# Kernel optimization log

Hardware: AMD Instinct MI355X
Metric: run time of the kernel (lower is better)

The kernel has to match this reference:

```python
import jax, jax.numpy as jnp
import numpy as np

N = 20000       # nodes
E = 320000      # edges (before self-loops)
F_IN = 1024     # num_features
H = 4           # head_num
C = 64          # hidden_size
NC = 4          # n_classes
NEG_SLOPE = 0.2 # PyG GATConv default


def setup_inputs() -> dict:
    key = jax.random.key(0)
    ks = jax.random.split(key, 16)
    def w(k, shape, fan_in):
        return jax.random.normal(k, shape, dtype=jnp.float32) / np.sqrt(fan_in)
    x = jax.random.normal(ks[0], (N, F_IN), dtype=jnp.float32)
    edge_index = jax.random.randint(ks[1], (2, E), 0, N, dtype=jnp.int64)
    return {
        "x": x,
        "edge_index": edge_index,
        # layer 1: F_IN -> H*C, concat
        "w1": w(ks[2], (F_IN, H * C), F_IN),
        "as1": w(ks[3], (H, C), C),
        "ad1": w(ks[4], (H, C), C),
        "b1": jnp.zeros((H * C,), jnp.float32),
        # layer 2: H*C -> H*C, concat
        "w2": w(ks[5], (H * C, H * C), H * C),
        "as2": w(ks[6], (H, C), C),
        "ad2": w(ks[7], (H, C), C),
        "b2": jnp.zeros((H * C,), jnp.float32),
        # out layer: H*C -> C, 1 head, concat=False
        "w3": w(ks[8], (H * C, 1 * C), H * C),
        "as3": w(ks[9], (1, C), C),
        "ad3": w(ks[10], (1, C), C),
        "b3": jnp.zeros((C,), jnp.float32),
        # classifier
        "wc": w(ks[11], (C, NC), C),
        "bc": jnp.zeros((NC,), jnp.float32),
    }


def gat_layer(x, src, dst, W, a_src, a_dst, bias, concat):
    """PyG GATConv (eval mode, self-loops already added to src/dst)."""
    n = x.shape[0]
    Hh, Cc = a_src.shape
    h = (x @ W).reshape(n, Hh, Cc)                       # [N,H,C]
    al_s = jnp.sum(h * a_src[None], axis=-1)             # [N,H]
    al_d = jnp.sum(h * a_dst[None], axis=-1)             # [N,H]
    e = al_s[src] + al_d[dst]                            # [E,H]
    e = jax.nn.leaky_relu(e, NEG_SLOPE)
    # segment softmax over incoming edges of each destination node
    emax = jax.ops.segment_max(e, dst, num_segments=n)   # [N,H]
    ex = jnp.exp(e - emax[dst])
    denom = jax.ops.segment_sum(ex, dst, num_segments=n) # [N,H]
    alpha = ex / (denom[dst] + 1e-16)                    # [E,H]
    msg = h[src] * alpha[..., None]                      # [E,H,C]
    out = jax.ops.segment_sum(msg, dst, num_segments=n)  # [N,H,C]
    if concat:
        out = out.reshape(n, Hh * Cc)
    else:
        out = out.mean(axis=1)
    return out + bias


def reference(x, edge_index, w1, as1, ad1, b1, w2, as2, ad2, b2,
              w3, as3, ad3, b3, wc, bc):
    n = x.shape[0]
    loop = jnp.arange(n, dtype=edge_index.dtype)
    src = jnp.concatenate([edge_index[0], loop])
    dst = jnp.concatenate([edge_index[1], loop])
    out = jax.nn.relu(gat_layer(x, src, dst, w1, as1, ad1, b1, True))
    out = jax.nn.relu(gat_layer(out, src, dst, w2, as2, ad2, b2, True))
    out = gat_layer(out, src, dst, w3, as3, ad3, b3, False)
    return out @ wc + bc                                  # [N, n_classes]
```

## Files before the change

### kernel.cpp

```cpp
#include <hip/hip_runtime.h>

#define N_NODES 20000
#define N_EDGES 320000
#define ET (N_EDGES + N_NODES)
#define F_IN 1024
#define HC 256
#define NC 4

typedef unsigned short ushort_t;
typedef __attribute__((ext_vector_type(8))) short short8;
typedef __attribute__((ext_vector_type(4))) float f32x4;

__device__ inline ushort_t f2bf(float f) {
    unsigned u = __float_as_uint(f);
    unsigned r = (u + 0x7fffu + ((u >> 16) & 1u)) >> 16;
    return (ushort_t)r;
}
__device__ inline float bf2f(ushort_t u) {
    return __uint_as_float(((unsigned)u) << 16);
}

__device__ inline unsigned cvt_pk_bf16(float lo, float hi) {
    unsigned r;
    asm("v_cvt_pk_bf16_f32 %0, %1, %2" : "=v"(r) : "v"(lo), "v"(hi));
    return r;
}

#define GLOAD16(gp, lp) __builtin_amdgcn_global_load_lds( \
    (const __attribute__((address_space(1))) void*)(gp),  \
    (__attribute__((address_space(3))) void*)(lp), 16, 0, 0)

__global__ void count_kernel(const int* __restrict__ ei, int* __restrict__ counts) {
    int e = blockIdx.x * blockDim.x + threadIdx.x;
    if (e >= ET) return;
    int dst = (e < N_EDGES) ? ei[N_EDGES + e] : (e - N_EDGES);
    atomicAdd(&counts[dst], 1);
}

__global__ void scan_kernel(const int* __restrict__ counts, int* __restrict__ row_ptr,
                            int* __restrict__ cursor) {
    __shared__ int sums[1024];
    int t = threadIdx.x;
    const int per = (N_NODES + 1023) / 1024;
    int b = t * per;
    int e = min(b + per, N_NODES);
    int s = 0;
    for (int i = b; i < e; ++i) s += counts[i];
    sums[t] = s;
    __syncthreads();
    for (int off = 1; off < 1024; off <<= 1) {
        int v = (t >= off) ? sums[t - off] : 0;
        __syncthreads();
        sums[t] += v;
        __syncthreads();
    }
    int run = (t == 0) ? 0 : sums[t - 1];
    for (int i = b; i < e; ++i) {
        row_ptr[i] = run;
        cursor[i]  = run;
        run += counts[i];
    }
    if (t == 0) row_ptr[N_NODES] = ET;
}

__global__ void scatter_kernel(const int* __restrict__ ei, int* __restrict__ cursor,
                               int* __restrict__ col) {
    int e = blockIdx.x * blockDim.x + threadIdx.x;
    if (e >= ET) return;
    int src, dst;
    if (e < N_EDGES) { src = ei[e]; dst = ei[N_EDGES + e]; }
    else             { src = dst = e - N_EDGES; }
    int pos = atomicAdd(&cursor[dst], 1);
    col[pos] = src;
}

__global__ void split_T(const float* __restrict__ in, ushort_t* __restrict__ hi,
                        ushort_t* __restrict__ lo, int K, int Nn) {
    int idx = blockIdx.x * blockDim.x + threadIdx.x;
    if (idx >= K * Nn) return;
    int k = idx / Nn, n = idx - k * Nn;
    float v = in[idx];
    ushort_t h = f2bf(v);
    hi[(size_t)n * K + k] = h;
    lo[(size_t)n * K + k] = f2bf(v - bf2f(h));
}

#define AL_EPILOGUE()                                                              \
    {                                                                              \
        float asv[NF], adv[NF];                                                    \
        _Pragma("unroll")                                                          \
        for (int j = 0; j < NF; ++j) {                                             \
            int col = bn + wn * SN + j * 16 + (lane & 15);                         \
            asv[j] = as_w[col];                                                    \
            adv[j] = ad_w[col];                                                    \
        }                                                                          \
        float* s_as = (float*)smem;                                   \
        float* s_ad = (float*)smem + 2 * BM;                                       \
        _Pragma("unroll")                                                          \
        for (int i = 0; i < MF; ++i) {                                             \
            _Pragma("unroll")                                                      \
            for (int rr = 0; rr < 4; ++rr) {                                       \
                float ps = 0.f, pd = 0.f;                                          \
                _Pragma("unroll")                                                  \
                for (int j = 0; j < NF; ++j) {                                     \
                    ps += acc[i][j][rr] * asv[j];                                  \
                    pd += acc[i][j][rr] * adv[j];                                  \
                }                                                                  \
                _Pragma("unroll")                                                  \
                for (int o = 1; o < 16; o <<= 1) {                                 \
                    ps += __shfl_xor(ps, o, 64);                                   \
                    pd += __shfl_xor(pd, o, 64);                                   \
                }                                                                  \
                if ((lane & 15) == 0) {                                            \
                    int rl = wm * SM + i * 16 + (lane >> 4) * 4 + rr;              \
                    s_as[wn * BM + rl] = ps;                                       \
                    s_ad[wn * BM + rl] = pd;                                       \
                }                                                                  \
            }                                                                      \
        }                                                                          \
        __syncthreads();                                                           \
        if (t < BM) {                                                              \
            int row = bm + t;                                                      \
            if (row < M) {                                                         \
                int hb = bn >> 6;                                                  \
                als[row * H + hb] = s_as[t] + s_as[BM + t];                        \
                ald[row * H + hb] = s_ad[t] + s_ad[BM + t];                        \
            }                                                                      \
        }                                                                          \
    }

template<int GY>
__launch_bounds__(256)
__global__ void gemm_f32a_ks(const float* __restrict__ X,
                             const ushort_t* __restrict__ BTh, const ushort_t* __restrict__ BTl,
                             float* __restrict__ Cp0, float* __restrict__ Cp1,
                             int M, int K, int NT) {
    constexpr int BM = 128, BN = 64, SM = 64, SN = 32, MF = 4, NF = 2;
    __shared__ __align__(16) char smem[49152];

    const int t = threadIdx.x, lane = t & 63, w = t >> 6;
    const int wm = w >> 1, wn = w & 1;
    const int nwg = gridDim.x;
    const int id = blockIdx.x;
    const int q = nwg >> 3, r = nwg & 7;
    const int xcd = id & 7, idx = id >> 3;
    const int logical = (xcd < r ? xcd * (q + 1) : r * (q + 1) + (xcd - r) * q) + idx;
    const int nwg_half = nwg >> 1;
    const int ks = logical / nwg_half;
    const int rem = logical - ks * nwg_half;
    const int bm = (rem / GY) * BM, bn = (rem % GY) * BN;
    const int kbase = ks * (K >> 1);
    float* Cp = ks ? Cp1 : Cp0;

    const int achk = lane & 3;
    const float* xRow[2]; int aoff[2];
    #pragma unroll
    for (int qq = 0; qq < 2; ++qq) {
        int arow = (w * 2 + qq) * 16 + (lane >> 2);
        int grow = min(bm + arow, M - 1);
        xRow[qq] = X + (size_t)grow * K + kbase + achk * 8;
        aoff[qq] = arow * 64 + ((achk ^ ((arow >> 1) & 3)) * 16);
    }
    const int gchunk = ((lane & 3) ^ ((lane >> 3) & 3)) * 16;
    const int brow = w * 16 + (lane >> 2);
    const size_t gB = (size_t)(bn + brow) * K * 2 + (size_t)kbase * 2 + gchunk;
    const int lB = w * 1024;

    const char* Bhb = (const char*)BTh;
    const char* Blb = (const char*)BTl;
    const int c16 = (lane >> 4);
    const int NTs = K >> 7;

    f32x4 acc[MF][NF];
    #pragma unroll
    for (int i = 0; i < MF; ++i)
        #pragma unroll
        for (int j = 0; j < NF; ++j) acc[i][j] = (f32x4){0.f, 0.f, 0.f, 0.f};

    float4 cur0[2][2], cur1[2][2], nxt0[2][2], nxt1[2][2];
    #pragma unroll
    for (int qq = 0; qq < 2; ++qq)
        #pragma unroll
        for (int kc = 0; kc < 2; ++kc) {
            cur0[qq][kc] = *(const float4*)(xRow[qq] + kc * 32);
            cur1[qq][kc] = *(const float4*)(xRow[qq] + kc * 32 + 4);
        }

    for (int ts = 0; ts < NTs; ++ts) {
        size_t kb = (size_t)ts * 128;
        #pragma unroll
        for (int kc = 0; kc < 2; ++kc) {
            GLOAD16(Bhb + gB + kb + kc * 64, smem + 32768 + kc * 4096 + lB);
            GLOAD16(Blb + gB + kb + kc * 64, smem + 40960 + kc * 4096 + lB);
        }
        #pragma unroll
        for (int qq = 0; qq < 2; ++qq)
            #pragma unroll
            for (int kc = 0; kc < 2; ++kc) {
                float vv[8] = {cur0[qq][kc].x, cur0[qq][kc].y, cur0[qq][kc].z, cur0[qq][kc].w,
                               cur1[qq][kc].x, cur1[qq][kc].y, cur1[qq][kc].z, cur1[qq][kc].w};
                unsigned hp[4], lp[4];
                #pragma unroll
                for (int j = 0; j < 4; ++j) {
                    unsigned h = cvt_pk_bf16(vv[2 * j], vv[2 * j + 1]);
                    float h0 = __uint_as_float(h << 16);
                    float h1 = __uint_as_float(h & 0xFFFF0000u);
                    hp[j] = h;
                    lp[j] = cvt_pk_bf16(vv[2 * j] - h0, vv[2 * j + 1] - h1);
                }
                *(uint4*)(smem + kc * 8192 + aoff[qq])         = make_uint4(hp[0], hp[1], hp[2], hp[3]);
                *(uint4*)(smem + 16384 + kc * 8192 + aoff[qq]) = make_uint4(lp[0], lp[1], lp[2], lp[3]);
            }
        __syncthreads();
        if (ts + 1 < NTs) {
            int ko = (ts + 1) * 64;
            #pragma unroll
            for (int qq = 0; qq < 2; ++qq)
                #pragma unroll
                for (int kc = 0; kc < 2; ++kc) {
                    nxt0[qq][kc] = *(const float4*)(xRow[qq] + ko + kc * 32);
                    nxt1[qq][kc] = *(const float4*)(xRow[qq] + ko + kc * 32 + 4);
                }
        }
        #pragma unroll
        for (int kc = 0; kc < 2; ++kc) {
            short8 afh[MF], afl[MF], bfh[NF], bfl[NF];
            #pragma unroll
            for (int i = 0; i < MF; ++i) {
                int row = wm * SM + i * 16 + (lane & 15);
                int off = row * 64 + ((c16 ^ ((row >> 1) & 3)) * 16);
                afh[i] = *(const short8*)(smem + kc * 8192 + off);
                afl[i] = *(const short8*)(smem + 16384 + kc * 8192 + off);
            }
            #pragma unroll
            for (int j = 0; j < NF; ++j) {
                int row = wn * SN + j * 16 + (lane & 15);
                int off = row * 64 + ((c16 ^ ((row >> 1) & 3)) * 16);
                bfh[j] = *(const short8*)(smem + 32768 + kc * 4096 + off);
                bfl[j] = *(const short8*)(smem + 40960 + kc * 4096 + off);
            }
            #pragma unroll
            for (int i = 0; i < MF; ++i)
                #pragma unroll
                for (int j = 0; j < NF; ++j) {
                    acc[i][j] = __builtin_amdgcn_mfma_f32_16x16x32_bf16(afh[i], bfh[j], acc[i][j], 0, 0, 0);
                    acc[i][j] = __builtin_amdgcn_mfma_f32_16x16x32_bf16(afh[i], bfl[j], acc[i][j], 0, 0, 0);
                    acc[i][j] = __builtin_amdgcn_mfma_f32_16x16x32_bf16(afl[i], bfh[j], acc[i][j], 0, 0, 0);
                }
        }
        __syncthreads();
        #pragma unroll
        for (int qq = 0; qq < 2; ++qq)
            #pragma unroll
            for (int kc = 0; kc < 2; ++kc) { cur0[qq][kc] = nxt0[qq][kc]; cur1[qq][kc] = nxt1[qq][kc]; }
    }
    #pragma unroll
    for (int i = 0; i < MF; ++i) {
        int rbase = bm + wm * SM + i * 16 + (lane >> 4) * 4;
        #pragma unroll
        for (int j = 0; j < NF; ++j) {
            int col = bn + wn * SN + j * 16 + (lane & 15);
            #pragma unroll
            for (int rr = 0; rr < 4; ++rr)
                if (rbase + rr < M) Cp[(size_t)(rbase + rr) * NT + col] = acc[i][j][rr];
        }
    }
}

__launch_bounds__(256)
__global__ void reduce_al(float* __restrict__ B0, const float* __restrict__ Cp1,
                          const float* __restrict__ as_w, const float* __restrict__ ad_w,
                          float* __restrict__ als, float* __restrict__ ald) {
    int lane = threadIdx.x & 63, w = threadIdx.x >> 6;
    int row = blockIdx.x * 4 + w;
    if (row >= N_NODES) return;
    size_t base = (size_t)row * HC + lane * 4;
    float4 p0 = *(const float4*)&B0[base];
    float4 p1 = *(const float4*)&Cp1[base];
    float4 s = make_float4(p0.x + p1.x, p0.y + p1.y, p0.z + p1.z, p0.w + p1.w);
    *(float4*)&B0[base] = s;
    int head = lane >> 4;
    int cw = (lane & 15) * 4;
    float ps = s.x * as_w[head * 64 + cw + 0] + s.y * as_w[head * 64 + cw + 1]
             + s.z * as_w[head * 64 + cw + 2] + s.w * as_w[head * 64 + cw + 3];
    float pd = s.x * ad_w[head * 64 + cw + 0] + s.y * ad_w[head * 64 + cw + 1]
             + s.z * ad_w[head * 64 + cw + 2] + s.w * ad_w[head * 64 + cw + 3];
    #pragma unroll
    for (int o = 1; o < 16; o <<= 1) {
        ps += __shfl_xor(ps, o, 64);
        pd += __shfl_xor(pd, o, 64);
    }
    if ((lane & 15) == 0) {
        als[row * 4 + head] = ps;
        ald[row * 4 + head] = pd;
    }
}

template<int BMT, int GY, int H>
__launch_bounds__(256)
__global__ void gemm_mfma(const ushort_t* __restrict__ Ah, const ushort_t* __restrict__ Al,
                          const ushort_t* __restrict__ BTh, const ushort_t* __restrict__ BTl,
                          float* __restrict__ C, const float* __restrict__ as_w,
                          const float* __restrict__ ad_w, float* __restrict__ als,
                          float* __restrict__ ald, int M, int K, int NT) {
    constexpr int BM = BMT, BN = 64, SM = BM / 2, SN = 32, MF = SM / 16, NF = 2;
    constexpr int AQ = BM / 64;
    constexpr int ASZ = BM * 64;
    __shared__ __align__(16) char smem[4 * ASZ + 16384];

    const int t = threadIdx.x, lane = t & 63, w = t >> 6;
    const int wm = w >> 1, wn = w & 1;
    const int nwg = gridDim.x;
    const int id = blockIdx.x;
    const int q = nwg >> 3, r = nwg & 7;
    const int xcd = id & 7, idx = id >> 3;
    const int logical = (xcd < r ? xcd * (q + 1) : r * (q + 1) + (xcd - r) * q) + idx;
    const int bm = (logical / GY) * BM, bn = (logical % GY) * BN;
    const int gchunk = ((lane & 3) ^ ((lane >> 3) & 3)) * 16;

    size_t gA[AQ]; int lA[AQ];
    #pragma unroll
    for (int qq = 0; qq < AQ; ++qq) {
        int inst = w * AQ + qq;
        int arow = inst * 16 + (lane >> 2);
        int grow = min(bm + arow, M - 1);
        gA[qq] = (size_t)grow * K * 2 + gchunk;
        lA[qq] = inst * 1024;
    }
    const int brow = w * 16 + (lane >> 2);
    const size_t gB = (size_t)(bn + brow) * K * 2 + gchunk;
    const int lB = w * 1024;

    const char* Ahb = (const char*)Ah;
    const char* Alb = (const char*)Al;
    const char* Bhb = (const char*)BTh;
    const char* Blb = (const char*)BTl;
    const int c16 = (lane >> 4);
    const int NTs = K / 64;

    f32x4 acc[MF][NF];
    #pragma unroll
    for (int i = 0; i < MF; ++i)
        #pragma unroll
        for (int j = 0; j < NF; ++j) acc[i][j] = (f32x4){0.f, 0.f, 0.f, 0.f};

    for (int ts = 0; ts < NTs; ++ts) {
        size_t kb = (size_t)ts * 128;
        #pragma unroll
        for (int kc = 0; kc < 2; ++kc) {
            #pragma unroll
            for (int qq = 0; qq < AQ; ++qq) {
                GLOAD16(Ahb + gA[qq] + kb + kc * 64, smem + kc * ASZ + lA[qq]);
                GLOAD16(Alb + gA[qq] + kb + kc * 64, smem + 2 * ASZ + kc * ASZ + lA[qq]);
            }
            GLOAD16(Bhb + gB + kb + kc * 64, smem + 4 * ASZ + kc * 4096 + lB);
            GLOAD16(Blb + gB + kb + kc * 64, smem + 4 * ASZ + 8192 + kc * 4096 + lB);
        }
        __syncthreads();
        #pragma unroll
        for (int kc = 0; kc < 2; ++kc) {
            short8 afh[MF], afl[MF], bfh[NF], bfl[NF];
            #pragma unroll
            for (int i = 0; i < MF; ++i) {
                int row = wm * SM + i * 16 + (lane & 15);
                int off = row * 64 + ((c16 ^ ((row >> 1) & 3)) * 16);
                afh[i] = *(const short8*)(smem + kc * ASZ + off);
                afl[i] = *(const short8*)(smem + 2 * ASZ + kc * ASZ + off);
            }
            #pragma unroll
            for (int j = 0; j < NF; ++j) {
                int row = wn * SN + j * 16 + (lane & 15);
                int off = row * 64 + ((c16 ^ ((row >> 1) & 3)) * 16);
                bfh[j] = *(const short8*)(smem + 4 * ASZ + kc * 4096 + off);
                bfl[j] = *(const short8*)(smem + 4 * ASZ + 8192 + kc * 4096 + off);
            }
            #pragma unroll
            for (int i = 0; i < MF; ++i)
                #pragma unroll
                for (int j = 0; j < NF; ++j) {
                    acc[i][j] = __builtin_amdgcn_mfma_f32_16x16x32_bf16(afh[i], bfh[j], acc[i][j], 0, 0, 0);
                    acc[i][j] = __builtin_amdgcn_mfma_f32_16x16x32_bf16(afh[i], bfl[j], acc[i][j], 0, 0, 0);
                    acc[i][j] = __builtin_amdgcn_mfma_f32_16x16x32_bf16(afl[i], bfh[j], acc[i][j], 0, 0, 0);
                }
        }
        __syncthreads();
    }
    #pragma unroll
    for (int i = 0; i < MF; ++i) {
        int rbase = bm + wm * SM + i * 16 + (lane >> 4) * 4;
        #pragma unroll
        for (int j = 0; j < NF; ++j) {
            int col = bn + wn * SN + j * 16 + (lane & 15);
            #pragma unroll
            for (int rr = 0; rr < 4; ++rr)
                if (rbase + rr < M) C[(size_t)(rbase + rr) * NT + col] = acc[i][j][rr];
        }
    }
    AL_EPILOGUE()
}

template<int CT, int CW, int H, bool RELU, bool SPLIT, bool CLS>
__launch_bounds__(256)
__global__ void agg_v6(const float* __restrict__ h, const float* __restrict__ als,
                       const float* __restrict__ ald,
                       const int* __restrict__ row_ptr, const int* __restrict__ col,
                       const float* __restrict__ bias,
                       ushort_t* __restrict__ oh, ushort_t* __restrict__ ol,
                       float* __restrict__ of,
                       const float* __restrict__ wc, const float* __restrict__ bc,
                       float* __restrict__ cls_out) {
    constexpr int NS  = CT / CW;
    constexpr int LPT = CW / 4;
    constexpr int TPW = 64 / LPT;
    static_assert(NS == H, "slice==head mapping");
    __shared__ int   s_src[4][64];
    __shared__ float s_alp[4][64];
    const int nwg = gridDim.x;
    const int q = nwg >> 3;
    int id = blockIdx.x;
    int logical = (id & 7) * q + (id >> 3);
    int slice = logical / (N_NODES / 4);
    int g = logical - slice * (N_NODES / 4);
    int lane = threadIdx.x & 63, w = threadIdx.x >> 6;
    int dst = g * 4 + w;
    int beg = row_ptr[dst], deg = row_ptr[dst + 1] - beg;
    int team = lane / LPT;
    int cc = (lane & (LPT - 1)) * 4;

    const int*   colP = col + beg;
    const float* hS   = h + slice * CW + cc;
    float ad = ald[dst * H + slice];

    float m = -1e30f, den = 0.f;
    for (int base = 0; base < deg; base += 64) {
        int i = base + lane;
        if (i < deg) {
            float e = als[colP[i] * H + slice] + ad;
            e = (e > 0.f) ? e : 0.2f * e;
            float nm = fmaxf(m, e);
            den = den * __expf(m - nm) + __expf(e - nm);
            m = nm;
        }
    }
    #pragma unroll
    for (int off = 1; off < 64; off <<= 1) {
        float mo = __shfl_xor(m, off, 64);
        float dn = __shfl_xor(den, off, 64);
        float nm = fmaxf(m, mo);
        den = den * __expf(m - nm) + dn * __expf(mo - nm);
        m = nm;
    }
    float rden = 1.f / (den + 1e-16f);

    float4 a0v = make_float4(0.f, 0.f, 0.f, 0.f);
    float4 a1v = make_float4(0.f, 0.f, 0.f, 0.f);
    float4 a2v = make_float4(0.f, 0.f, 0.f, 0.f);
    float4 a3v = make_float4(0.f, 0.f, 0.f, 0.f);
    for (int base = 0; base < deg; base += 64) {
        int cnt = min(64, deg - base);
        if (lane < cnt) {
            int src = colP[base + lane];
            s_src[w][lane] = src;
            float e = als[src * H + slice] + ad;
            e = (e > 0.f) ? e : 0.2f * e;
            s_alp[w][lane] = __expf(e - m) * rden;
        }
        int i = team;
        for (; i + 3 * TPW < cnt; i += 4 * TPW) {
            int   s0 = s_src[w][i],           s1 = s_src[w][i + TPW];
            int   s2 = s_src[w][i + 2 * TPW], s3 = s_src[w][i + 3 * TPW];
            float a0 = s_alp[w][i],           a1 = s_alp[w][i + TPW];
            float a2 = s_alp[w][i + 2 * TPW], a3 = s_alp[w][i + 3 * TPW];
            float4 h0 = *(const float4*)&hS[s0 * CT];
            float4 h1 = *(const float4*)&hS[s1 * CT];
            float4 h2 = *(const float4*)&hS[s2 * CT];
            float4 h3 = *(const float4*)&hS[s3 * CT];
            a0v.x += a0 * h0.x; a0v.y += a0 * h0.y; a0v.z += a0 * h0.z; a0v.w += a0 * h0.w;
            a1v.x += a1 * h1.x; a1v.y += a1 * h1.y; a1v.z += a1 * h1.z; a1v.w += a1 * h1.w;
            a2v.x += a2 * h2.x; a2v.y += a2 * h2.y; a2v.z += a2 * h2.z; a2v.w += a2 * h2.w;
            a3v.x += a3 * h3.x; a3v.y += a3 * h3.y; a3v.z += a3 * h3.z; a3v.w += a3 * h3.w;
        }
        for (; i < cnt; i += TPW) {
            int   s0 = s_src[w][i];
            float a0 = s_alp[w][i];
            float4 h0 = *(const float4*)&hS[s0 * CT];
            a0v.x += a0 * h0.x; a0v.y += a0 * h0.y; a0v.z += a0 * h0.z; a0v.w += a0 * h0.w;
        }
    }
    float4 acc = make_float4((a0v.x + a1v.x) + (a2v.x + a3v.x),
                             (a0v.y + a1v.y) + (a2v.y + a3v.y),
                             (a0v.z + a1v.z) + (a2v.z + a3v.z),
                             (a0v.w + a1v.w) + (a2v.w + a3v.w));
    #pragma unroll
    for (int off = LPT; off < 64; off <<= 1) {
        acc.x += __shfl_xor(acc.x, off, 64);
        acc.y += __shfl_xor(acc.y, off, 64);
        acc.z += __shfl_xor(acc.z, off, 64);
        acc.w += __shfl_xor(acc.w, off, 64);
    }
    if (team == 0) {
        int ch = slice * CW + cc;
        float4 bv = *(const float4*)&bias[ch];
        float v0 = acc.x + bv.x, v1 = acc.y + bv.y, v2 = acc.z + bv.z, v3 = acc.w + bv.w;
        if (RELU) {
            v0 = fmaxf(v0, 0.f); v1 = fmaxf(v1, 0.f);
            v2 = fmaxf(v2, 0.f); v3 = fmaxf(v3, 0.f);
        }
        if (CLS) {
            float ps[NC];
            #pragma unroll
            for (int k = 0; k < NC; ++k)
                ps[k] = v0 * wc[(cc + 0) * NC + k] + v1 * wc[(cc + 1) * NC + k]
                      + v2 * wc[(cc + 2) * NC + k] + v3 * wc[(cc + 3) * NC + k];
            #pragma unroll
            for (int o = 1; o < 16; o <<= 1)
                #pragma unroll
                for (int k = 0; k < NC; ++k) ps[k] += __shfl_xor(ps[k], o, 64);
            if (lane == 0) {
                #pragma unroll
                for (int k = 0; k < NC; ++k) cls_out[(size_t)dst * NC + k] = ps[k] + bc[k];
            }
        } else {
            size_t idx = (size_t)dst * CT + ch;
            if (SPLIT) {
                ushort4 h4, l4;
                h4.x = f2bf(v0); l4.x = f2bf(v0 - bf2f(h4.x));
                h4.y = f2bf(v1); l4.y = f2bf(v1 - bf2f(h4.y));
                h4.z = f2bf(v2); l4.z = f2bf(v2 - bf2f(h4.z));
                h4.w = f2bf(v3); l4.w = f2bf(v3 - bf2f(h4.w));
                *(ushort4*)&oh[idx] = h4;
                *(ushort4*)&ol[idx] = l4;
            } else {
                *(float4*)&of[idx] = make_float4(v0, v1, v2, v3);
            }
        }
    }
}

extern "C" void kernel_launch(void* const* d_in, const int* in_sizes, int n_in,
                              void* d_out, int out_size, void* d_ws, size_t ws_size,
                              hipStream_t stream) {
    const float* x   = (const float*)d_in[0];
    const int*   ei  = (const int*)d_in[1];
    const float* w1  = (const float*)d_in[2];
    const float* as1 = (const float*)d_in[3];
    const float* ad1 = (const float*)d_in[4];
    const float* b1  = (const float*)d_in[5];
    const float* w2  = (const float*)d_in[6];
    const float* as2 = (const float*)d_in[7];
    const float* ad2 = (const float*)d_in[8];
    const float* b2  = (const float*)d_in[9];
    const float* w3  = (const float*)d_in[10];
    const float* as3 = (const float*)d_in[11];
    const float* ad3 = (const float*)d_in[12];
    const float* b3  = (const float*)d_in[13];
    const float* wc  = (const float*)d_in[14];
    const float* bc  = (const float*)d_in[15];
    float* out = (float*)d_out;

    char* ws = (char*)d_ws;
    size_t off = 0;
    auto alloc = [&](size_t bytes) -> char* {
        char* p = ws + off;
        off = (off + bytes + 255) & ~(size_t)255;
        return p;
    };

    int* counts  = (int*)alloc(N_NODES * 4);
    int* cursor  = (int*)alloc(N_NODES * 4);
    int* row_ptr = (int*)alloc((N_NODES + 1) * 4);
    int* colidx  = (int*)alloc(ET * 4);
    float* als   = (float*)alloc(N_NODES * 4 * 4);
    float* ald   = (float*)alloc(N_NODES * 4 * 4);
    float* B0    = (float*)alloc((size_t)N_NODES * HC * 4);
    float* Cp1   = (float*)alloc((size_t)N_NODES * HC * 4);

    ushort_t* w1Th = (ushort_t*)alloc((size_t)F_IN * HC * 2);
    ushort_t* w1Tl = (ushort_t*)alloc((size_t)F_IN * HC * 2);
    ushort_t* w2Th = (ushort_t*)alloc((size_t)HC * HC * 2);
    ushort_t* w2Tl = (ushort_t*)alloc((size_t)HC * HC * 2);
    ushort_t* w3Th = (ushort_t*)alloc((size_t)HC * 64 * 2);
    ushort_t* w3Tl = (ushort_t*)alloc((size_t)HC * 64 * 2);
    ushort_t* B1h  = (ushort_t*)alloc((size_t)N_NODES * HC * 2);
    ushort_t* B1l  = (ushort_t*)alloc((size_t)N_NODES * HC * 2);

    hipMemsetAsync(counts, 0, N_NODES * sizeof(int), stream);
    int eb = (ET + 255) / 256;
    count_kernel<<<eb, 256, 0, stream>>>(ei, counts);
    scan_kernel<<<1, 1024, 0, stream>>>(counts, row_ptr, cursor);
    scatter_kernel<<<eb, 256, 0, stream>>>(ei, cursor, colidx);

    split_T<<<(F_IN * HC + 255) / 256, 256, 0, stream>>>(w1, w1Th, w1Tl, F_IN, HC);
    split_T<<<(HC * HC + 255) / 256, 256, 0, stream>>>(w2, w2Th, w2Tl, HC, HC);
    split_T<<<(HC * 64 + 255) / 256, 256, 0, stream>>>(w3, w3Th, w3Tl, HC, 64);

    const int nwg128 = ((N_NODES + 127) / 128) * (HC / 64);
    const int nblk_dst = N_NODES / 4;
    gemm_f32a_ks<4><<<2 * nwg128, 256, 0, stream>>>(x, w1Th, w1Tl, B0, Cp1, N_NODES, F_IN, HC);
    reduce_al<<<nblk_dst, 256, 0, stream>>>(B0, Cp1, as1, ad1, als, ald);
    agg_v6<256, 64, 4, true, true, false><<<4 * nblk_dst, 256, 0, stream>>>(
        B0, als, ald, row_ptr, colidx, b1, B1h, B1l, nullptr, nullptr, nullptr, nullptr);
    gemm_mfma<128, 4, 4><<<nwg128, 256, 0, stream>>>(B1h, B1l, w2Th, w2Tl, B0, as2, ad2,
                                                     als, ald, N_NODES, HC, HC);
    agg_v6<256, 64, 4, true, true, false><<<4 * nblk_dst, 256, 0, stream>>>(
        B0, als, ald, row_ptr, colidx, b2, B1h, B1l, nullptr, nullptr, nullptr, nullptr);
    const int nwg3 = (N_NODES + 63) / 64;
    gemm_mfma<64, 1, 1><<<nwg3, 256, 0, stream>>>(B1h, B1l, w3Th, w3Tl, B0, as3, ad3,
                                                  als, ald, N_NODES, HC, 64);
    agg_v6<64, 64, 1, false, false, true><<<nblk_dst, 256, 0, stream>>>(
        B0, als, ald, row_ptr, colidx, b3, nullptr, nullptr, nullptr, wc, bc, out);
}
```

Before: 285.2 us.

## Merge graph preprocessing and weight splitting into fewer heterogeneous kernel launches

```diff
diff --git a/kernel.cpp b/kernel.cpp
--- a/kernel.cpp
+++ b/kernel.cpp
@@ -30,59 +30,255 @@
     (const __attribute__((address_space(1))) void*)(gp),  \
     (__attribute__((address_space(3))) void*)(lp), 16, 0, 0)
 
-__global__ void count_kernel(const int* __restrict__ ei, int* __restrict__ counts) {
-    int e = blockIdx.x * blockDim.x + threadIdx.x;
-    if (e >= ET) return;
-    int dst = (e < N_EDGES) ? ei[N_EDGES + e] : (e - N_EDGES);
-    atomicAdd(&counts[dst], 1);
-}
-
-__global__ void scan_kernel(const int* __restrict__ counts, int* __restrict__ row_ptr,
-                            int* __restrict__ cursor) {
-    __shared__ int sums[1024];
-    int t = threadIdx.x;
-    const int per = (N_NODES + 1023) / 1024;
-    int b = t * per;
-    int e = min(b + per, N_NODES);
-    int s = 0;
-    for (int i = b; i < e; ++i) s += counts[i];
-    sums[t] = s;
-    __syncthreads();
-    for (int off = 1; off < 1024; off <<= 1) {
-        int v = (t >= off) ? sums[t - off] : 0;
+__global__ void d1_split1_count(const float* __restrict__ w1, ushort_t* __restrict__ w1Th,
+                                ushort_t* __restrict__ w1Tl,
+                                const int* __restrict__ ei, int* __restrict__ counts) {
+    const int S1 = F_IN * HC / 256;
+    int b = blockIdx.x;
+    if (b < S1) {
+        int idx = b * 256 + threadIdx.x;
+        int k = idx / HC, n = idx - k * HC;
+        float v = w1[idx];
+        ushort_t h = f2bf(v);
+        w1Th[(size_t)n * F_IN + k] = h;
+        w1Tl[(size_t)n * F_IN + k] = f2bf(v - bf2f(h));
+    } else {
+        int e = (b - S1) * 256 + threadIdx.x;
+        if (e < ET) {
+            int dst = (e < N_EDGES) ? ei[N_EDGES + e] : (e - N_EDGES);
+            atomicAdd(&counts[dst], 1);
+        }
+    }
+}
+
+template<int GY>
+__launch_bounds__(256)
+__global__ void d2_gemm1_fused(const float* __restrict__ X,
+                               const ushort_t* __restrict__ BTh, const ushort_t* __restrict__ BTl,
+                               float* __restrict__ Cp0, float* __restrict__ Cp1,
+                               int M, int K, int NT, int nwgG,
+                               const int* __restrict__ counts, int* __restrict__ row_ptr,
+                               int* __restrict__ cursor,
+                               const float* __restrict__ w2, ushort_t* __restrict__ w2Th,
+                               ushort_t* __restrict__ w2Tl,
+                               const float* __restrict__ w3, ushort_t* __restrict__ w3Th,
+                               ushort_t* __restrict__ w3Tl) {
+    constexpr int BM = 128, BN = 64, SM = 64, SN = 32, MF = 4, NF = 2;
+    __shared__ __align__(16) char smem[49152];
+
+    const int bid = blockIdx.x;
+    if (bid >= nwgG) {
+        int rb = bid - nwgG;
+        if (rb == 0) {
+            int* ssum = (int*)smem;
+            int tt = threadIdx.x;
+            const int per = (N_NODES + 255) / 256;
+            int b0 = tt * per, e0 = min(b0 + per, N_NODES);
+            int s = 0;
+            for (int i = b0; i < e0; ++i) s += counts[i];
+            ssum[tt] = s;
+            __syncthreads();
+            for (int o = 1; o < 256; o <<= 1) {
+                int v = (tt >= o) ? ssum[tt - o] : 0;
+                __syncthreads();
+                ssum[tt] += v;
+                __syncthreads();
+            }
+            int run = (tt == 0) ? 0 : ssum[tt - 1];
+            for (int i = b0; i < e0; ++i) {
+                row_ptr[i] = run;
+                cursor[i]  = run;
+                run += counts[i];
+            }
+            if (tt == 0) row_ptr[N_NODES] = ET;
+        } else if (rb <= 256) {
+            int idx = (rb - 1) * 256 + threadIdx.x;
+            int k = idx / HC, n = idx - k * HC;
+            float v = w2[idx];
+            ushort_t h = f2bf(v);
+            w2Th[(size_t)n * HC + k] = h;
+            w2Tl[(size_t)n * HC + k] = f2bf(v - bf2f(h));
+        } else {
+            int idx = (rb - 257) * 256 + threadIdx.x;
+            int k = idx / 64, n = idx - k * 64;
+            float v = w3[idx];
+            ushort_t h = f2bf(v);
+            w3Th[(size_t)n * HC + k] = h;
+            w3Tl[(size_t)n * HC + k] = f2bf(v - bf2f(h));
+        }
+        return;
+    }
+
+    const int t = threadIdx.x, lane = t & 63, w = t >> 6;
+    const int wm = w >> 1, wn = w & 1;
+    const int nwg = nwgG;
+    const int id = bid;
+    const int q = nwg >> 3, r = nwg & 7;
+    const int xcd = id & 7, idx = id >> 3;
+    const int logical = (xcd < r ? xcd * (q + 1) : r * (q + 1) + (xcd - r) * q) + idx;
+    const int nwg_half = nwg >> 1;
+    const int ks = logical / nwg_half;
+    const int rem = logical - ks * nwg_half;
+    const int bm = (rem / GY) * BM, bn = (rem % GY) * BN;
+    const int kbase = ks * (K >> 1);
+    float* Cp = ks ? Cp1 : Cp0;
+
+    const int achk = lane & 3;
+    const float* xRow[2]; int aoff[2];
+    #pragma unroll
+    for (int qq = 0; qq < 2; ++qq) {
+        int arow = (w * 2 + qq) * 16 + (lane >> 2);
+        int grow = min(bm + arow, M - 1);
+        xRow[qq] = X + (size_t)grow * K + kbase + achk * 8;
+        aoff[qq] = arow * 64 + ((achk ^ ((arow >> 1) & 3)) * 16);
+    }
+    const int gchunk = ((lane & 3) ^ ((lane >> 3) & 3)) * 16;
+    const int brow = w * 16 + (lane >> 2);
+    const size_t gB = (size_t)(bn + brow) * K * 2 + (size_t)kbase * 2 + gchunk;
+    const int lB = w * 1024;
+
+    const char* Bhb = (const char*)BTh;
+    const char* Blb = (const char*)BTl;
+    const int c16 = (lane >> 4);
+    const int NTs = K >> 7;
+
+    f32x4 acc[MF][NF];
+    #pragma unroll
+    for (int i = 0; i < MF; ++i)
+        #pragma unroll
+        for (int j = 0; j < NF; ++j) acc[i][j] = (f32x4){0.f, 0.f, 0.f, 0.f};
+
+    float4 cur0[2][2], cur1[2][2], nxt0[2][2], nxt1[2][2];
+    #pragma unroll
+    for (int qq = 0; qq < 2; ++qq)
+        #pragma unroll
+        for (int kc = 0; kc < 2; ++kc) {
+            cur0[qq][kc] = *(const float4*)(xRow[qq] + kc * 32);
+            cur1[qq][kc] = *(const float4*)(xRow[qq] + kc * 32 + 4);
+        }
+
+    for (int ts = 0; ts < NTs; ++ts) {
+        size_t kb = (size_t)ts * 128;
+        #pragma unroll
+        for (int kc = 0; kc < 2; ++kc) {
+            GLOAD16(Bhb + gB + kb + kc * 64, smem + 32768 + kc * 4096 + lB);
+            GLOAD16(Blb + gB + kb + kc * 64, smem + 40960 + kc * 4096 + lB);
+        }
+        #pragma unroll
+        for (int qq = 0; qq < 2; ++qq)
+            #pragma unroll
+            for (int kc = 0; kc < 2; ++kc) {
+                float vv[8] = {cur0[qq][kc].x, cur0[qq][kc].y, cur0[qq][kc].z, cur0[qq][kc].w,
+                               cur1[qq][kc].x, cur1[qq][kc].y, cur1[qq][kc].z, cur1[qq][kc].w};
+                unsigned hp[4], lp[4];
+                #pragma unroll
+                for (int j = 0; j < 4; ++j) {
+                    unsigned h = cvt_pk_bf16(vv[2 * j], vv[2 * j + 1]);
+                    float h0 = __uint_as_float(h << 16);
+                    float h1 = __uint_as_float(h & 0xFFFF0000u);
+                    hp[j] = h;
+                    lp[j] = cvt_pk_bf16(vv[2 * j] - h0, vv[2 * j + 1] - h1);
+                }
+                *(uint4*)(smem + kc * 8192 + aoff[qq])         = make_uint4(hp[0], hp[1], hp[2], hp[3]);
+                *(uint4*)(smem + 16384 + kc * 8192 + aoff[qq]) = make_uint4(lp[0], lp[1], lp[2], lp[3]);
+            }
         __syncthreads();
-        sums[t] += v;
+        if (ts + 1 < NTs) {
+            int ko = (ts + 1) * 64;
+            #pragma unroll
+            for (int qq = 0; qq < 2; ++qq)
+                #pragma unroll
+                for (int kc = 0; kc < 2; ++kc) {
+                    nxt0[qq][kc] = *(const float4*)(xRow[qq] + ko + kc * 32);
+                    nxt1[qq][kc] = *(const float4*)(xRow[qq] + ko + kc * 32 + 4);
+                }
+        }
+        #pragma unroll
+        for (int kc = 0; kc < 2; ++kc) {
+            short8 afh[MF], afl[MF], bfh[NF], bfl[NF];
+            #pragma unroll
+            for (int i = 0; i < MF; ++i) {
+                int row = wm * SM + i * 16 + (lane & 15);
+                int off = row * 64 + ((c16 ^ ((row >> 1) & 3)) * 16);
+                afh[i] = *(const short8*)(smem + kc * 8192 + off);
+                afl[i] = *(const short8*)(smem + 16384 + kc * 8192 + off);
+            }
+            #pragma unroll
+            for (int j = 0; j < NF; ++j) {
+                int row = wn * SN + j * 16 + (lane & 15);
+                int off = row * 64 + ((c16 ^ ((row >> 1) & 3)) * 16);
+                bfh[j] = *(const short8*)(smem + 32768 + kc * 4096 + off);
+                bfl[j] = *(const short8*)(smem + 40960 + kc * 4096 + off);
+            }
+            #pragma unroll
+            for (int i = 0; i < MF; ++i)
+                #pragma unroll
+                for (int j = 0; j < NF; ++j) {
+                    acc[i][j] = __builtin_amdgcn_mfma_f32_16x16x32_bf16(afh[i], bfh[j], acc[i][j], 0, 0, 0);
+                    acc[i][j] = __builtin_amdgcn_mfma_f32_16x16x32_bf16(afh[i], bfl[j], acc[i][j], 0, 0, 0);
+                    acc[i][j] = __builtin_amdgcn_mfma_f32_16x16x32_bf16(afl[i], bfh[j], acc[i][j], 0, 0, 0);
+                }
+        }
         __syncthreads();
-    }
-    int run = (t == 0) ? 0 : sums[t - 1];
-    for (int i = b; i < e; ++i) {
-        row_ptr[i] = run;
-        cursor[i]  = run;
-        run += counts[i];
-    }
-    if (t == 0) row_ptr[N_NODES] = ET;
-}
-
-__global__ void scatter_kernel(const int* __restrict__ ei, int* __restrict__ cursor,
-                               int* __restrict__ col) {
-    int e = blockIdx.x * blockDim.x + threadIdx.x;
-    if (e >= ET) return;
-    int src, dst;
-    if (e < N_EDGES) { src = ei[e]; dst = ei[N_EDGES + e]; }
-    else             { src = dst = e - N_EDGES; }
-    int pos = atomicAdd(&cursor[dst], 1);
-    col[pos] = src;
-}
-
-__global__ void split_T(const float* __restrict__ in, ushort_t* __restrict__ hi,
-                        ushort_t* __restrict__ lo, int K, int Nn) {
-    int idx = blockIdx.x * blockDim.x + threadIdx.x;
-    if (idx >= K * Nn) return;
-    int k = idx / Nn, n = idx - k * Nn;
-    float v = in[idx];
-    ushort_t h = f2bf(v);
-    hi[(size_t)n * K + k] = h;
-    lo[(size_t)n * K + k] = f2bf(v - bf2f(h));
+        #pragma unroll
+        for (int qq = 0; qq < 2; ++qq)
+            #pragma unroll
+            for (int kc = 0; kc < 2; ++kc) { cur0[qq][kc] = nxt0[qq][kc]; cur1[qq][kc] = nxt1[qq][kc]; }
+    }
+    #pragma unroll
+    for (int i = 0; i < MF; ++i) {
+        int rbase = bm + wm * SM + i * 16 + (lane >> 4) * 4;
+        #pragma unroll
+        for (int j = 0; j < NF; ++j) {
+            int col = bn + wn * SN + j * 16 + (lane & 15);
+            #pragma unroll
+            for (int rr = 0; rr < 4; ++rr)
+                if (rbase + rr < M) Cp[(size_t)(rbase + rr) * NT + col] = acc[i][j][rr];
+        }
+    }
+}
+
+__launch_bounds__(256)
+__global__ void d3_scatter_reduce(const int* __restrict__ ei, int* __restrict__ cursor,
+                                  int* __restrict__ col,
+                                  float* __restrict__ B0, const float* __restrict__ Cp1,
+                                  const float* __restrict__ as_w, const float* __restrict__ ad_w,
+                                  float* __restrict__ als, float* __restrict__ ald) {
+    const int EB = (ET + 255) / 256;
+    int b = blockIdx.x;
+    if (b < EB) {
+        int e = b * 256 + threadIdx.x;
+        if (e >= ET) return;
+        int src, dst;
+        if (e < N_EDGES) { src = ei[e]; dst = ei[N_EDGES + e]; }
+        else             { src = dst = e - N_EDGES; }
+        int pos = atomicAdd(&cursor[dst], 1);
+        col[pos] = src;
+        return;
+    }
+    int lane = threadIdx.x & 63, w = threadIdx.x >> 6;
+    int row = (b - EB) * 4 + w;
+    if (row >= N_NODES) return;
+    size_t base = (size_t)row * HC + lane * 4;
+    float4 p0 = *(const float4*)&B0[base];
+    float4 p1 = *(const float4*)&Cp1[base];
+    float4 s = make_float4(p0.x + p1.x, p0.y + p1.y, p0.z + p1.z, p0.w + p1.w);
+    *(float4*)&B0[base] = s;
+    int head = lane >> 4;
+    int cw = (lane & 15) * 4;
+    float ps = s.x * as_w[head * 64 + cw + 0] + s.y * as_w[head * 64 + cw + 1]
+             + s.z * as_w[head * 64 + cw + 2] + s.w * as_w[head * 64 + cw + 3];
+    float pd = s.x * ad_w[head * 64 + cw + 0] + s.y * ad_w[head * 64 + cw + 1]
+             + s.z * ad_w[head * 64 + cw + 2] + s.w * ad_w[head * 64 + cw + 3];
+    #pragma unroll
+    for (int o = 1; o < 16; o <<= 1) {
+        ps += __shfl_xor(ps, o, 64);
+        pd += __shfl_xor(pd, o, 64);
+    }
+    if ((lane & 15) == 0) {
+        als[row * 4 + head] = ps;
+        ald[row * 4 + head] = pd;
+    }
 }
 
 #define AL_EPILOGUE()                                                              \
@@ -129,173 +325,6 @@
         }                                                                          \
     }
 
-template<int GY>
-__launch_bounds__(256)
-__global__ void gemm_f32a_ks(const float* __restrict__ X,
-                             const ushort_t* __restrict__ BTh, const ushort_t* __restrict__ BTl,
-                             float* __restrict__ Cp0, float* __restrict__ Cp1,
-                             int M, int K, int NT) {
-    constexpr int BM = 128, BN = 64, SM = 64, SN = 32, MF = 4, NF = 2;
-    __shared__ __align__(16) char smem[49152];
-
-    const int t = threadIdx.x, lane = t & 63, w = t >> 6;
-    const int wm = w >> 1, wn = w & 1;
-    const int nwg = gridDim.x;
-    const int id = blockIdx.x;
-    const int q = nwg >> 3, r = nwg & 7;
-    const int xcd = id & 7, idx = id >> 3;
-    const int logical = (xcd < r ? xcd * (q + 1) : r * (q + 1) + (xcd - r) * q) + idx;
-    const int nwg_half = nwg >> 1;
-    const int ks = logical / nwg_half;
-    const int rem = logical - ks * nwg_half;
-    const int bm = (rem / GY) * BM, bn = (rem % GY) * BN;
-    const int kbase = ks * (K >> 1);
-    float* Cp = ks ? Cp1 : Cp0;
-
-    const int achk = lane & 3;
-    const float* xRow[2]; int aoff[2];
-    #pragma unroll
-    for (int qq = 0; qq < 2; ++qq) {
-        int arow = (w * 2 + qq) * 16 + (lane >> 2);
-        int grow = min(bm + arow, M - 1);
-        xRow[qq] = X + (size_t)grow * K + kbase + achk * 8;
-        aoff[qq] = arow * 64 + ((achk ^ ((arow >> 1) & 3)) * 16);
-    }
-    const int gchunk = ((lane & 3) ^ ((lane >> 3) & 3)) * 16;
-    const int brow = w * 16 + (lane >> 2);
-    const size_t gB = (size_t)(bn + brow) * K * 2 + (size_t)kbase * 2 + gchunk;
-    const int lB = w * 1024;
-
-    const char* Bhb = (const char*)BTh;
-    const char* Blb = (const char*)BTl;
-    const int c16 = (lane >> 4);
-    const int NTs = K >> 7;
-
-    f32x4 acc[MF][NF];
-    #pragma unroll
-    for (int i = 0; i < MF; ++i)
-        #pragma unroll
-        for (int j = 0; j < NF; ++j) acc[i][j] = (f32x4){0.f, 0.f, 0.f, 0.f};
-
-    float4 cur0[2][2], cur1[2][2], nxt0[2][2], nxt1[2][2];
-    #pragma unroll
-    for (int qq = 0; qq < 2; ++qq)
-        #pragma unroll
-        for (int kc = 0; kc < 2; ++kc) {
-            cur0[qq][kc] = *(const float4*)(xRow[qq] + kc * 32);
-            cur1[qq][kc] = *(const float4*)(xRow[qq] + kc * 32 + 4);
-        }
-
-    for (int ts = 0; ts < NTs; ++ts) {
-        size_t kb = (size_t)ts * 128;
-        #pragma unroll
-        for (int kc = 0; kc < 2; ++kc) {
-            GLOAD16(Bhb + gB + kb + kc * 64, smem + 32768 + kc * 4096 + lB);
-            GLOAD16(Blb + gB + kb + kc * 64, smem + 40960 + kc * 4096 + lB);
-        }
-        #pragma unroll
-        for (int qq = 0; qq < 2; ++qq)
-            #pragma unroll
-            for (int kc = 0; kc < 2; ++kc) {
-                float vv[8] = {cur0[qq][kc].x, cur0[qq][kc].y, cur0[qq][kc].z, cur0[qq][kc].w,
-                               cur1[qq][kc].x, cur1[qq][kc].y, cur1[qq][kc].z, cur1[qq][kc].w};
-                unsigned hp[4], lp[4];
-                #pragma unroll
-                for (int j = 0; j < 4; ++j) {
-                    unsigned h = cvt_pk_bf16(vv[2 * j], vv[2 * j + 1]);
-                    float h0 = __uint_as_float(h << 16);
-                    float h1 = __uint_as_float(h & 0xFFFF0000u);
-                    hp[j] = h;
-                    lp[j] = cvt_pk_bf16(vv[2 * j] - h0, vv[2 * j + 1] - h1);
-                }
-                *(uint4*)(smem + kc * 8192 + aoff[qq])         = make_uint4(hp[0], hp[1], hp[2], hp[3]);
-                *(uint4*)(smem + 16384 + kc * 8192 + aoff[qq]) = make_uint4(lp[0], lp[1], lp[2], lp[3]);
-            }
-        __syncthreads();
-        if (ts + 1 < NTs) {
-            int ko = (ts + 1) * 64;
-            #pragma unroll
-            for (int qq = 0; qq < 2; ++qq)
-                #pragma unroll
-                for (int kc = 0; kc < 2; ++kc) {
-                    nxt0[qq][kc] = *(const float4*)(xRow[qq] + ko + kc * 32);
-                    nxt1[qq][kc] = *(const float4*)(xRow[qq] + ko + kc * 32 + 4);
-                }
-        }
-        #pragma unroll
-        for (int kc = 0; kc < 2; ++kc) {
-            short8 afh[MF], afl[MF], bfh[NF], bfl[NF];
-            #pragma unroll
-            for (int i = 0; i < MF; ++i) {
-                int row = wm * SM + i * 16 + (lane & 15);
-                int off = row * 64 + ((c16 ^ ((row >> 1) & 3)) * 16);
-                afh[i] = *(const short8*)(smem + kc * 8192 + off);
-                afl[i] = *(const short8*)(smem + 16384 + kc * 8192 + off);
-            }
-            #pragma unroll
-            for (int j = 0; j < NF; ++j) {
-                int row = wn * SN + j * 16 + (lane & 15);
-                int off = row * 64 + ((c16 ^ ((row >> 1) & 3)) * 16);
-                bfh[j] = *(const short8*)(smem + 32768 + kc * 4096 + off);
-                bfl[j] = *(const short8*)(smem + 40960 + kc * 4096 + off);
-            }
-            #pragma unroll
-            for (int i = 0; i < MF; ++i)
-                #pragma unroll
-                for (int j = 0; j < NF; ++j) {
-                    acc[i][j] = __builtin_amdgcn_mfma_f32_16x16x32_bf16(afh[i], bfh[j], acc[i][j], 0, 0, 0);
-                    acc[i][j] = __builtin_amdgcn_mfma_f32_16x16x32_bf16(afh[i], bfl[j], acc[i][j], 0, 0, 0);
-                    acc[i][j] = __builtin_amdgcn_mfma_f32_16x16x32_bf16(afl[i], bfh[j], acc[i][j], 0, 0, 0);
-                }
-        }
-        __syncthreads();
-        #pragma unroll
-        for (int qq = 0; qq < 2; ++qq)
-            #pragma unroll
-            for (int kc = 0; kc < 2; ++kc) { cur0[qq][kc] = nxt0[qq][kc]; cur1[qq][kc] = nxt1[qq][kc]; }
-    }
-    #pragma unroll
-    for (int i = 0; i < MF; ++i) {
-        int rbase = bm + wm * SM + i * 16 + (lane >> 4) * 4;
-        #pragma unroll
-        for (int j = 0; j < NF; ++j) {
-            int col = bn + wn * SN + j * 16 + (lane & 15);
-            #pragma unroll
-            for (int rr = 0; rr < 4; ++rr)
-                if (rbase + rr < M) Cp[(size_t)(rbase + rr) * NT + col] = acc[i][j][rr];
-        }
-    }
-}
-
-__launch_bounds__(256)
-__global__ void reduce_al(float* __restrict__ B0, const float* __restrict__ Cp1,
-                          const float* __restrict__ as_w, const float* __restrict__ ad_w,
-                          float* __restrict__ als, float* __restrict__ ald) {
-    int lane = threadIdx.x & 63, w = threadIdx.x >> 6;
-    int row = blockIdx.x * 4 + w;
-    if (row >= N_NODES) return;
-    size_t base = (size_t)row * HC + lane * 4;
-    float4 p0 = *(const float4*)&B0[base];
-    float4 p1 = *(const float4*)&Cp1[base];
-    float4 s = make_float4(p0.x + p1.x, p0.y + p1.y, p0.z + p1.z, p0.w + p1.w);
-    *(float4*)&B0[base] = s;
-    int head = lane >> 4;
-    int cw = (lane & 15) * 4;
-    float ps = s.x * as_w[head * 64 + cw + 0] + s.y * as_w[head * 64 + cw + 1]
-             + s.z * as_w[head * 64 + cw + 2] + s.w * as_w[head * 64 + cw + 3];
-    float pd = s.x * ad_w[head * 64 + cw + 0] + s.y * ad_w[head * 64 + cw + 1]
-             + s.z * ad_w[head * 64 + cw + 2] + s.w * ad_w[head * 64 + cw + 3];
-    #pragma unroll
-    for (int o = 1; o < 16; o <<= 1) {
-        ps += __shfl_xor(ps, o, 64);
-        pd += __shfl_xor(pd, o, 64);
-    }
-    if ((lane & 15) == 0) {
-        als[row * 4 + head] = ps;
-        ald[row * 4 + head] = pd;
-    }
-}
-
 template<int BMT, int GY, int H>
 __launch_bounds__(256)
 __global__ void gemm_mfma(const ushort_t* __restrict__ Ah, const ushort_t* __restrict__ Al,
@@ -584,20 +613,19 @@
     ushort_t* B1h  = (ushort_t*)alloc((size_t)N_NODES * HC * 2);
     ushort_t* B1l  = (ushort_t*)alloc((size_t)N_NODES * HC * 2);
 
+    const int EB = (ET + 255) / 256;
+    const int S1 = F_IN * HC / 256;
+    const int nwg128 = ((N_NODES + 127) / 128) * (HC / 64);
+    const int nwgG = 2 * nwg128;
+    const int nblk_dst = N_NODES / 4;
+
     hipMemsetAsync(counts, 0, N_NODES * sizeof(int), stream);
-    int eb = (ET + 255) / 256;
-    count_kernel<<<eb, 256, 0, stream>>>(ei, counts);
-    scan_kernel<<<1, 1024, 0, stream>>>(counts, row_ptr, cursor);
-    scatter_kernel<<<eb, 256, 0, stream>>>(ei, cursor, colidx);
-
-    split_T<<<(F_IN * HC + 255) / 256, 256, 0, stream>>>(w1, w1Th, w1Tl, F_IN, HC);
-    split_T<<<(HC * HC + 255) / 256, 256, 0, stream>>>(w2, w2Th, w2Tl, HC, HC);
-    split_T<<<(HC * 64 + 255) / 256, 256, 0, stream>>>(w3, w3Th, w3Tl, HC, 64);
-
-    const int nwg128 = ((N_NODES + 127) / 128) * (HC / 64);
-    const int nblk_dst = N_NODES / 4;
-    gemm_f32a_ks<4><<<2 * nwg128, 256, 0, stream>>>(x, w1Th, w1Tl, B0, Cp1, N_NODES, F_IN, HC);
-    reduce_al<<<nblk_dst, 256, 0, stream>>>(B0, Cp1, as1, ad1, als, ald);
+    d1_split1_count<<<S1 + EB, 256, 0, stream>>>(w1, w1Th, w1Tl, ei, counts);
+    d2_gemm1_fused<4><<<nwgG + 1 + 256 + 64, 256, 0, stream>>>(
+        x, w1Th, w1Tl, B0, Cp1, N_NODES, F_IN, HC, nwgG,
+        counts, row_ptr, cursor, w2, w2Th, w2Tl, w3, w3Th, w3Tl);
+    d3_scatter_reduce<<<EB + nblk_dst, 256, 0, stream>>>(
+        ei, cursor, colidx, B0, Cp1, as1, ad1, als, ald);
     agg_v6<256, 64, 4, true, true, false><<<4 * nblk_dst, 256, 0, stream>>>(
         B0, als, ald, row_ptr, colidx, b1, B1h, B1l, nullptr, nullptr, nullptr, nullptr);
     gemm_mfma<128, 4, 4><<<nwg128, 256, 0, stream>>>(B1h, B1l, w2Th, w2Tl, B0, as2, ad2,
```

Measured after the change: 277.5 us. 1.03x faster.
